# Optimization experiments

Measured on AMD Instinct MI355X. Metric: run time of the kernel, lower is better.

The kernel has to match this reference:

```python
import jax, jax.numpy as jnp
import numpy as np

EPS = 1e-5
B, N, NODE_DIM, D, H, DK, FF, L = 16, 512, 2, 256, 8, 32, 512, 3


def _u(key, shape):
    s = 1.0 / np.sqrt(shape[-1])
    return jax.random.uniform(key, shape, minval=-s, maxval=s, dtype=jnp.float32)


def _bn(h, g, b):
    # BatchNorm1d in training mode over flattened (B*N, D): biased variance
    m = h.mean(axis=(0, 1))
    v = h.var(axis=(0, 1))
    return (h - m) / jnp.sqrt(v + EPS) * g + b


def _edge_bias(em, eW1, eb1, eW2, eb2, eW3, eb3):
    # MLP(1, [16,16,H]) applied to each scalar edge weight -> (H, B, N, N)
    e = em[..., None]                       # (B,N,N,1)
    t = jax.nn.relu(e @ eW1 + eb1)          # (B,N,N,16)
    t = jax.nn.relu(t @ eW2 + eb2)          # (B,N,N,16)
    t = t @ eW3 + eb3                       # (B,N,N,H)
    return jnp.transpose(t, (3, 0, 1, 2))   # (H,B,N,N)


def _mha(h, Wq, Wk, Wv, Wo, bias):
    dk = Wq.shape[-1]
    Q = jnp.einsum('bnd,hdk->hbnk', h, Wq)
    K = jnp.einsum('bnd,hdk->hbnk', h, Wk)
    V = jnp.einsum('bnd,hdk->hbnk', h, Wv)
    scores = jnp.einsum('hbqk,hbnk->hbqn', Q, K) * (1.0 / jnp.sqrt(jnp.asarray(dk, h.dtype)))
    if bias is not None:
        scores = scores + bias
    attn = jax.nn.softmax(scores, axis=-1)
    heads = jnp.einsum('hbqn,hbnk->hbqk', attn, V)
    return jnp.einsum('hbqk,hke->bqe', heads, Wo)


def setup_inputs() -> dict:
    key = jax.random.key(0)
    ks = jax.random.split(key, 24)
    inp = {
        'x': jax.random.normal(ks[0], (B, N, NODE_DIM), dtype=jnp.float32),
        'edge_matrix': jax.random.uniform(ks[1], (B, N, N), dtype=jnp.float32),
        'init_W': _u(ks[2], (NODE_DIM, D)),
        'init_b': _u(ks[3], (D,)),
        'Wq': _u(ks[4], (L, H, D, DK)),
        'Wk': _u(ks[5], (L, H, D, DK)),
        'Wv': _u(ks[6], (L, H, D, DK)),
        'Wo': _u(ks[7], (L, H, DK, D)),
        'eW1': _u(ks[8], (1, 16)),
        'eb1': _u(ks[9], (16,)),
        'eW2': _u(ks[10], (16, 16)),
        'eb2': _u(ks[11], (16,)),
        'eW3': _u(ks[12], (16, H)),
        'eb3': _u(ks[13], (H,)),
        'bn1_g': jnp.ones((L, D), jnp.float32),
        'bn1_b': jnp.zeros((L, D), jnp.float32),
        'ffW1': _u(ks[14], (L, D, FF)),
        'ffb1': _u(ks[15], (L, FF)),
        'ffW2': _u(ks[16], (L, FF, D)),
        'ffb2': _u(ks[17], (L, D)),
        'bn2_g': jnp.ones((L, D), jnp.float32),
        'bn2_b': jnp.zeros((L, D), jnp.float32),
    }
    return inp


def reference(x, edge_matrix, init_W, init_b, Wq, Wk, Wv, Wo,
              eW1, eb1, eW2, eb2, eW3, eb3,
              bn1_g, bn1_b, ffW1, ffb1, ffW2, ffb2, bn2_g, bn2_b):
    h = x @ init_W + init_b                          # init_embed: (B,N,D)
    bias0 = _edge_bias(edge_matrix, eW1, eb1, eW2, eb2, eW3, eb3)
    for l in range(L):
        b_l = bias0 if l < 1 else None               # n_edge_encode_layers = 1
        h = h + _mha(h, Wq[l], Wk[l], Wv[l], Wo[l], b_l)
        h = _bn(h, bn1_g[l], bn1_b[l])
        h = h + (jax.nn.relu(h @ ffW1[l] + ffb1[l]) @ ffW2[l] + ffb2[l])
        h = _bn(h, bn2_g[l], bn2_b[l])
    graph_embed = h.mean(axis=1)                     # add_graph_dim == 0
    return (h, graph_embed)
```

## Files before the change

### kernel.cpp

```cpp
#include <hip/hip_runtime.h>

#define BB    16
#define NNN   512
#define DDIM  256
#define HH    8
#define DKK   32
#define FFF   512
#define MROWS 8192
#define LUTN  4096

using u16    = unsigned short;
using bf16x8 = __attribute__((ext_vector_type(8))) short;
using f32x4  = __attribute__((ext_vector_type(4))) float;

__device__ __forceinline__ float bf2f(u16 u) { return __uint_as_float(((unsigned)u) << 16); }
__device__ __forceinline__ u16 f2bf(float f) {
    unsigned u = __float_as_uint(f);
    return (u16)((u + 0x7fffu + ((u >> 16) & 1u)) >> 16);
}

__global__ __launch_bounds__(256) void init_embed_kernel(
    const float* __restrict__ x, const float* __restrict__ W,
    const float* __restrict__ b, float* __restrict__ h)
{
    size_t row = blockIdx.x;
    int c = threadIdx.x;
    float x0 = x[row * 2 + 0], x1 = x[row * 2 + 1];
    h[row * DDIM + c] = x0 * W[c] + x1 * W[DDIM + c] + b[c];
}

__global__ __launch_bounds__(256) void build_lut_kernel(
    const float* __restrict__ eW1, const float* __restrict__ eb1,
    const float* __restrict__ eW2, const float* __restrict__ eb2,
    const float* __restrict__ eW3, const float* __restrict__ eb3,
    float* __restrict__ lut)
{
    int i = blockIdx.x * 256 + threadIdx.x;
    if (i > LUTN) return;
    float e = (float)i * (1.0f / LUTN);
    float t1[16], t2[16];
    #pragma unroll
    for (int a = 0; a < 16; ++a) t1[a] = fmaxf(e * eW1[a] + eb1[a], 0.0f);
    #pragma unroll
    for (int j = 0; j < 16; ++j) {
        float s = eb2[j];
        #pragma unroll
        for (int a = 0; a < 16; ++a) s += t1[a] * eW2[a * 16 + j];
        t2[j] = fmaxf(s, 0.0f);
    }
    #pragma unroll
    for (int hd = 0; hd < 8; ++hd) {
        float s = eb3[hd];
        #pragma unroll
        for (int j = 0; j < 16; ++j) s += t2[j] * eW3[j * 8 + hd];
        lut[(size_t)i * 8 + hd] = s;
    }
}

__global__ __launch_bounds__(256) void edge_bias_kernel(
    const float* __restrict__ edge, const float* __restrict__ lut,
    u16* __restrict__ bout)
{
    size_t idx = (size_t)blockIdx.x * 256 + threadIdx.x;
    float e = edge[idx];
    float f = e * (float)LUTN;
    f = fminf(fmaxf(f, 0.0f), (float)LUTN - 0.0001f);
    int i0 = (int)f;
    float fr = f - (float)i0;
    const float4* r = (const float4*)(lut + (size_t)i0 * 8);
    float4 a0 = r[0], a1 = r[1], b0 = r[2], b1 = r[3];
    float o[8];
    o[0] = a0.x + fr * (b0.x - a0.x);
    o[1] = a0.y + fr * (b0.y - a0.y);
    o[2] = a0.z + fr * (b0.z - a0.z);
    o[3] = a0.w + fr * (b0.w - a0.w);
    o[4] = a1.x + fr * (b1.x - a1.x);
    o[5] = a1.y + fr * (b1.y - a1.y);
    o[6] = a1.z + fr * (b1.z - a1.z);
    o[7] = a1.w + fr * (b1.w - a1.w);
    #pragma unroll
    for (int hd = 0; hd < 8; ++hd)
        bout[(size_t)hd * (size_t)BB * NNN * NNN + idx] = f2bf(o[hd]);
}

#define GBM 128
#define GBN 64
#define GBK 32
#define LPAD 40

template <int BMODE>
__global__ __launch_bounds__(256) void gemm_kernel(
    const float* __restrict__ A, int lda,
    const float* __restrict__ Bp, int ldb,
    const float* __restrict__ Wq, const float* __restrict__ Wk,
    const float* __restrict__ Wv, int layer,
    float* __restrict__ C, int ldc,
    const float* __restrict__ bias, int relu,
    const float* __restrict__ res, int ldr,
    int K)
{
    __shared__ u16 Ash[GBM][LPAD];
    __shared__ u16 Asl[GBM][LPAD];
    __shared__ u16 Bsh[GBN][LPAD];
    __shared__ u16 Bsl[GBN][LPAD];
    int m0 = blockIdx.y * GBM;
    int n0 = blockIdx.x * GBN;
    int tid = threadIdx.x;
    int lid = tid & 63, wid = tid >> 6;
    int wm = wid >> 1, wn = wid & 1;
    int l15 = lid & 15, l4 = lid >> 4;

    f32x4 acc[4][2] = {};

    for (int k0 = 0; k0 < K; k0 += GBK) {
        #pragma unroll
        for (int j = 0; j < 4; ++j) {
            int idx = tid + 256 * j;
            int row = idx >> 3, k4 = idx & 7;
            float4 v = *(const float4*)(A + (size_t)(m0 + row) * lda + k0 + k4 * 4);
            ushort4 wh, wl;
            wh.x = f2bf(v.x); wl.x = f2bf(v.x - bf2f(wh.x));
            wh.y = f2bf(v.y); wl.y = f2bf(v.y - bf2f(wh.y));
            wh.z = f2bf(v.z); wl.z = f2bf(v.z - bf2f(wh.z));
            wh.w = f2bf(v.w); wl.w = f2bf(v.w - bf2f(wh.w));
            *(ushort4*)&Ash[row][k4 * 4] = wh;
            *(ushort4*)&Asl[row][k4 * 4] = wl;
        }
        #pragma unroll
        for (int j = 0; j < 8; ++j) {
            int idx = tid + 256 * j;
            int kk = idx >> 6, nn = idx & 63;
            int gk = k0 + kk, gn = n0 + nn;
            float v;
            if (BMODE == 0) {
                v = Bp[(size_t)gk * ldb + gn];
            } else {
                int mat = gn >> 8, c8 = gn & 255, hd = c8 >> 5, dk = c8 & 31;
                const float* Wsel = (mat == 0) ? Wq : ((mat == 1) ? Wk : Wv);
                v = Wsel[(((size_t)layer * HH + hd) * DDIM + gk) * DKK + dk];
            }
            u16 hh = f2bf(v);
            Bsh[nn][kk] = hh;
            Bsl[nn][kk] = f2bf(v - bf2f(hh));
        }
        __syncthreads();
        bf16x8 afh[4], afl[4], bfh[2], bfl[2];
        #pragma unroll
        for (int mi = 0; mi < 4; ++mi) {
            afh[mi] = *(const bf16x8*)&Ash[wm * 64 + mi * 16 + l15][l4 * 8];
            afl[mi] = *(const bf16x8*)&Asl[wm * 64 + mi * 16 + l15][l4 * 8];
        }
        #pragma unroll
        for (int ni = 0; ni < 2; ++ni) {
            bfh[ni] = *(const bf16x8*)&Bsh[wn * 32 + ni * 16 + l15][l4 * 8];
            bfl[ni] = *(const bf16x8*)&Bsl[wn * 32 + ni * 16 + l15][l4 * 8];
        }
        #pragma unroll
        for (int mi = 0; mi < 4; ++mi)
            #pragma unroll
            for (int ni = 0; ni < 2; ++ni) {
                acc[mi][ni] = __builtin_amdgcn_mfma_f32_16x16x32_bf16(
                    afh[mi], bfh[ni], acc[mi][ni], 0, 0, 0);
                acc[mi][ni] = __builtin_amdgcn_mfma_f32_16x16x32_bf16(
                    afh[mi], bfl[ni], acc[mi][ni], 0, 0, 0);
                acc[mi][ni] = __builtin_amdgcn_mfma_f32_16x16x32_bf16(
                    afl[mi], bfh[ni], acc[mi][ni], 0, 0, 0);
            }
        __syncthreads();
    }
    #pragma unroll
    for (int mi = 0; mi < 4; ++mi) {
        #pragma unroll
        for (int ni = 0; ni < 2; ++ni) {
            #pragma unroll
            for (int r = 0; r < 4; ++r) {
                int row = m0 + wm * 64 + mi * 16 + l4 * 4 + r;
                int col = n0 + wn * 32 + ni * 16 + l15;
                float v = acc[mi][ni][r];
                if (bias) v += bias[col];
                if (relu) v = fmaxf(v, 0.0f);
                if (res)  v += res[(size_t)row * ldr + col];
                C[(size_t)row * ldc + col] = v;
            }
        }
    }
}

__global__ __launch_bounds__(512, 2) void attn_mfma_kernel(
    const float* __restrict__ qkv, const u16* __restrict__ bias,
    float* __restrict__ att)
{
    __shared__ u16 Ksh[512][32];
    __shared__ u16 Ksl[512][32];
    __shared__ u16 Vt[32][520];
    __shared__ u16 Pw[8][16][136];
    int wg = blockIdx.x;
    int logical = (wg & 7) * 64 + (wg >> 3);
    int qt = logical & 3, hd = (logical >> 2) & 7, b = logical >> 5;
    int tid = threadIdx.x, lid = tid & 63, w = tid >> 6;
    int l15 = lid & 15, l4 = lid >> 4;

    const float* base = qkv + (size_t)b * 512 * 768;
    for (int idx = tid; idx < 512 * 32; idx += 512) {
        int n = idx >> 5, k = idx & 31;
        float kv = base[(size_t)n * 768 + 256 + hd * 32 + k];
        u16 kh = f2bf(kv);
        Ksh[n][k] = kh;
        Ksl[n][k] = f2bf(kv - bf2f(kh));
        Vt[k][n] = f2bf(base[(size_t)n * 768 + 512 + hd * 32 + k]);
    }
    __syncthreads();

    int qw0 = qt * 128 + w * 16;
    bf16x8 afh, afl;
    {
        const float* qrow = base + (size_t)(qw0 + l15) * 768 + hd * 32 + l4 * 8;
        u16 th[8], tl[8];
        #pragma unroll
        for (int j = 0; j < 8; ++j) {
            float v = qrow[j];
            th[j] = f2bf(v);
            tl[j] = f2bf(v - bf2f(th[j]));
        }
        afh = *(bf16x8*)th;
        afl = *(bf16x8*)tl;
    }

    f32x4 acc[32];
    #pragma unroll
    for (int ct = 0; ct < 32; ++ct) {
        bf16x8 bh = *(const bf16x8*)&Ksh[ct * 16 + l15][l4 * 8];
        bf16x8 bl = *(const bf16x8*)&Ksl[ct * 16 + l15][l4 * 8];
        f32x4 z = {0.0f, 0.0f, 0.0f, 0.0f};
        z = __builtin_amdgcn_mfma_f32_16x16x32_bf16(afh, bh, z, 0, 0, 0);
        z = __builtin_amdgcn_mfma_f32_16x16x32_bf16(afl, bh, z, 0, 0, 0);
        acc[ct] = __builtin_amdgcn_mfma_f32_16x16x32_bf16(afh, bl, z, 0, 0, 0);
    }

    const float scale = 0.17677669529663687f;
    if (bias) {
        size_t brow = (((size_t)hd * BB + b) * NNN + qw0 + l4 * 4) * NNN + l15;
        #pragma unroll
        for (int ct = 0; ct < 32; ++ct)
            #pragma unroll
            for (int r = 0; r < 4; ++r)
                acc[ct][r] = acc[ct][r] * scale +
                             bf2f(bias[brow + (size_t)r * NNN + ct * 16]);
    } else {
        #pragma unroll
        for (int ct = 0; ct < 32; ++ct)
            #pragma unroll
            for (int r = 0; r < 4; ++r)
                acc[ct][r] *= scale;
    }

    float linv[4];
    #pragma unroll
    for (int r = 0; r < 4; ++r) {
        float m = acc[0][r];
        #pragma unroll
        for (int ct = 1; ct < 32; ++ct) m = fmaxf(m, acc[ct][r]);
        #pragma unroll
        for (int msk = 1; msk < 16; msk <<= 1) m = fmaxf(m, __shfl_xor(m, msk));
        float lsum = 0.0f;
        #pragma unroll
        for (int ct = 0; ct < 32; ++ct) {
            float p = __expf(acc[ct][r] - m);
            acc[ct][r] = p;
            lsum += p;
        }
        #pragma unroll
        for (int msk = 1; msk < 16; msk <<= 1) lsum += __shfl_xor(lsum, msk);
        linv[r] = 1.0f / lsum;
    }

    f32x4 oacc[2] = {};
    for (int cc = 0; cc < 4; ++cc) {
        #pragma unroll
        for (int ct8 = 0; ct8 < 8; ++ct8) {
            int ct = cc * 8 + ct8;
            #pragma unroll
            for (int r = 0; r < 4; ++r)
                Pw[w][l4 * 4 + r][ct8 * 16 + l15] = f2bf(acc[ct][r]);
        }
        #pragma unroll
        for (int ks = 0; ks < 4; ++ks) {
            bf16x8 pa = *(const bf16x8*)&Pw[w][l15][ks * 32 + l4 * 8];
            #pragma unroll
            for (int ct2 = 0; ct2 < 2; ++ct2) {
                bf16x8 vb = *(const bf16x8*)&Vt[ct2 * 16 + l15][cc * 128 + ks * 32 + l4 * 8];
                oacc[ct2] = __builtin_amdgcn_mfma_f32_16x16x32_bf16(pa, vb, oacc[ct2], 0, 0, 0);
            }
        }
    }
    #pragma unroll
    for (int ct2 = 0; ct2 < 2; ++ct2)
        #pragma unroll
        for (int r = 0; r < 4; ++r)
            att[((size_t)b * NNN + qw0 + l4 * 4 + r) * DDIM + hd * 32 + ct2 * 16 + l15] =
                oacc[ct2][r] * linv[r];
}

__global__ void zero_stats_kernel(float* stats)
{
    stats[threadIdx.x] = 0.0f;
    stats[256 + threadIdx.x] = 0.0f;
}

__global__ __launch_bounds__(256) void bn_stats_kernel(
    const float* __restrict__ X, float* __restrict__ stats)
{
    int c = threadIdx.x;
    size_t r0 = (size_t)blockIdx.x * 32;
    float s = 0.0f, ss = 0.0f;
    for (int r = 0; r < 32; ++r) {
        float v = X[(r0 + r) * DDIM + c];
        s += v; ss += v * v;
    }
    atomicAdd(&stats[c], s);
    atomicAdd(&stats[256 + c], ss);
}

__global__ __launch_bounds__(256) void bn_apply_kernel(
    const float* __restrict__ X, float* __restrict__ Y,
    const float* __restrict__ stats,
    const float* __restrict__ g, const float* __restrict__ bb)
{
    int c = threadIdx.x;
    float mean = stats[c] * (1.0f / MROWS);
    float var  = stats[256 + c] * (1.0f / MROWS) - mean * mean;
    float inv  = rsqrtf(var + 1e-5f);
    float gg = g[c] * inv;
    float off = bb[c] - mean * gg;
    size_t r0 = (size_t)blockIdx.x * 8;
    #pragma unroll
    for (int r = 0; r < 8; ++r) {
        size_t o = (r0 + r) * DDIM + c;
        Y[o] = X[o] * gg + off;
    }
}

__global__ __launch_bounds__(256) void graph_embed_kernel(
    const float* __restrict__ outh, float* __restrict__ outg)
{
    int c = threadIdx.x, b = blockIdx.x;
    float s = 0.0f;
    for (int n = 0; n < NNN; ++n)
        s += outh[((size_t)b * NNN + n) * DDIM + c];
    outg[b * DDIM + c] = s * (1.0f / NNN);
}

extern "C" void kernel_launch(void* const* d_in, const int* in_sizes, int n_in,
                              void* d_out, int out_size, void* d_ws, size_t ws_size,
                              hipStream_t stream)
{
    const float* x     = (const float*)d_in[0];
    const float* edge  = (const float*)d_in[1];
    const float* initW = (const float*)d_in[2];
    const float* initb = (const float*)d_in[3];
    const float* Wq    = (const float*)d_in[4];
    const float* Wk    = (const float*)d_in[5];
    const float* Wv    = (const float*)d_in[6];
    const float* Wo    = (const float*)d_in[7];
    const float* eW1   = (const float*)d_in[8];
    const float* eb1   = (const float*)d_in[9];
    const float* eW2   = (const float*)d_in[10];
    const float* eb2   = (const float*)d_in[11];
    const float* eW3   = (const float*)d_in[12];
    const float* eb3   = (const float*)d_in[13];
    const float* bn1g  = (const float*)d_in[14];
    const float* bn1b  = (const float*)d_in[15];
    const float* ffW1  = (const float*)d_in[16];
    const float* ffb1  = (const float*)d_in[17];
    const float* ffW2  = (const float*)d_in[18];
    const float* ffb2  = (const float*)d_in[19];
    const float* bn2g  = (const float*)d_in[20];
    const float* bn2b  = (const float*)d_in[21];

    char* ws = (char*)d_ws;
    float* h     = (float*)(ws);
    float* h2    = (float*)(ws + ((size_t)8 << 20));
    float* qkv   = (float*)(ws + ((size_t)16 << 20));
    float* attb  = (float*)(ws + ((size_t)40 << 20));
    float* ff    = (float*)(ws + ((size_t)48 << 20));
    float* stats = (float*)(ws + ((size_t)64 << 20));
    float* lut   = (float*)(ws + ((size_t)64 << 20) + 4096);
    u16*   bias  = (u16*)  (ws + ((size_t)65 << 20));
    float* outh  = (float*)d_out;
    float* outg  = outh + (size_t)MROWS * DDIM;

    init_embed_kernel<<<MROWS, 256, 0, stream>>>(x, initW, initb, h);
    build_lut_kernel<<<17, 256, 0, stream>>>(eW1, eb1, eW2, eb2, eW3, eb3, lut);
    edge_bias_kernel<<<(BB * NNN * NNN) / 256, 256, 0, stream>>>(edge, lut, bias);

    for (int l = 0; l < 3; ++l) {
        gemm_kernel<1><<<dim3(768 / GBN, MROWS / GBM), 256, 0, stream>>>(
            h, 256, nullptr, 0, Wq, Wk, Wv, l, qkv, 768,
            nullptr, 0, nullptr, 0, 256);
        attn_mfma_kernel<<<512, 512, 0, stream>>>(
            qkv, (l == 0) ? bias : (const u16*)nullptr, attb);
        gemm_kernel<0><<<dim3(256 / GBN, MROWS / GBM), 256, 0, stream>>>(
            attb, 256, Wo + (size_t)l * 256 * 256, 256,
            nullptr, nullptr, nullptr, 0, h2, 256,
            nullptr, 0, h, 256, 256);
        zero_stats_kernel<<<1, 256, 0, stream>>>(stats);
        bn_stats_kernel<<<256, 256, 0, stream>>>(h2, stats);
        bn_apply_kernel<<<1024, 256, 0, stream>>>(h2, h, stats, bn1g + l * 256, bn1b + l * 256);
        gemm_kernel<0><<<dim3(512 / GBN, MROWS / GBM), 256, 0, stream>>>(
            h, 256, ffW1 + (size_t)l * 256 * 512, 512,
            nullptr, nullptr, nullptr, 0, ff, 512,
            ffb1 + l * 512, 1, nullptr, 0, 256);
        gemm_kernel<0><<<dim3(256 / GBN, MROWS / GBM), 256, 0, stream>>>(
            ff, 512, ffW2 + (size_t)l * 512 * 256, 256,
            nullptr, nullptr, nullptr, 0, h2, 256,
            ffb2 + l * 256, 0, h, 256, 512);
        zero_stats_kernel<<<1, 256, 0, stream>>>(stats);
        bn_stats_kernel<<<256, 256, 0, stream>>>(h2, stats);
        bn_apply_kernel<<<1024, 256, 0, stream>>>(
            h2, (l == 2) ? outh : h, stats, bn2g + l * 256, bn2b + l * 256);
    }
    graph_embed_kernel<<<BB, 256, 0, stream>>>(outh, outg);
}
```

Before: 779.7 us.

## Pre-split activations and weights into bf16 hi/lo planes produced by upstream kernels

Producers (init embed, GEMM epilogues, attention output, BN apply) now write activations as separate bf16 hi/lo planes, and a one-time kernel pre-splits and transposes all weights into a K-contiguous bf16 layout. The new GEMM loads A as bf16 vectors into shared memory with a K tile of 64 and reads B fragments straight from global memory, so the repeated fp32-to-split conversion and the scalar B loads in every GEMM tile disappear. Attention reads the pre-split Q/K/V and reuses one shared buffer for Ksl and the P tiles, cutting LDS use. The cost is extra global writes of hi/lo planes and B reads from global/L2 in the GEMM without shared-memory staging.

```diff
diff --git a/kernel.cpp b/kernel.cpp
--- a/kernel.cpp
+++ b/kernel.cpp
@@ -21,12 +21,57 @@
 
 __global__ __launch_bounds__(256) void init_embed_kernel(
     const float* __restrict__ x, const float* __restrict__ W,
-    const float* __restrict__ b, float* __restrict__ h)
+    const float* __restrict__ b, float* __restrict__ h,
+    u16* __restrict__ hhi, u16* __restrict__ hlo)
 {
     size_t row = blockIdx.x;
     int c = threadIdx.x;
     float x0 = x[row * 2 + 0], x1 = x[row * 2 + 1];
-    h[row * DDIM + c] = x0 * W[c] + x1 * W[DDIM + c] + b[c];
+    float v = x0 * W[c] + x1 * W[DDIM + c] + b[c];
+    size_t o = row * DDIM + c;
+    h[o] = v;
+    u16 hv = f2bf(v);
+    hhi[o] = hv;
+    hlo[o] = f2bf(v - bf2f(hv));
+}
+
+#define WT_LSTR 1048576
+__global__ __launch_bounds__(256) void wsplit_kernel(
+    const float* __restrict__ Wq, const float* __restrict__ Wk,
+    const float* __restrict__ Wv, const float* __restrict__ Wo,
+    const float* __restrict__ ffW1, const float* __restrict__ ffW2,
+    u16* __restrict__ Wt)
+{
+    int fid = blockIdx.x * 256 + threadIdx.x;
+    int l = fid >> 19, r = fid & 524287;
+    u16* base = Wt + (size_t)l * WT_LSTR;
+    float v; int off_hi, off_lo;
+    if (r < 196608) {
+        int n = r >> 8, k = r & 255;
+        int mat = n >> 8, hd = (n & 255) >> 5, dk = n & 31;
+        const float* Wsel = (mat == 0) ? Wq : ((mat == 1) ? Wk : Wv);
+        v = Wsel[(((size_t)l * HH + hd) * DDIM + k) * DKK + dk];
+        off_hi = r; off_lo = r + 196608;
+    } else if (r < 262144) {
+        int r2 = r - 196608;
+        int n = r2 >> 8, k = r2 & 255;
+        int hd = k >> 5, dk = k & 31;
+        v = Wo[(((size_t)l * HH + hd) * DKK + dk) * DDIM + n];
+        off_hi = 393216 + r2; off_lo = 458752 + r2;
+    } else if (r < 393216) {
+        int r3 = r - 262144;
+        int n = r3 >> 8, k = r3 & 255;
+        v = ffW1[((size_t)l * DDIM + k) * FFF + n];
+        off_hi = 524288 + r3; off_lo = 655360 + r3;
+    } else {
+        int r4 = r - 393216;
+        int n = r4 >> 9, k = r4 & 511;
+        v = ffW2[((size_t)l * FFF + k) * DDIM + n];
+        off_hi = 786432 + r4; off_lo = 917504 + r4;
+    }
+    u16 hv = f2bf(v);
+    base[off_hi] = hv;
+    base[off_lo] = f2bf(v - bf2f(hv));
 }
 
 __global__ __launch_bounds__(256) void build_lut_kernel(
@@ -83,89 +128,61 @@
         bout[(size_t)hd * (size_t)BB * NNN * NNN + idx] = f2bf(o[hd]);
 }
 
-#define GBM 128
-#define GBN 64
-#define GBK 32
-#define LPAD 40
-
-template <int BMODE>
-__global__ __launch_bounds__(256) void gemm_kernel(
-    const float* __restrict__ A, int lda,
-    const float* __restrict__ Bp, int ldb,
-    const float* __restrict__ Wq, const float* __restrict__ Wk,
-    const float* __restrict__ Wv, int layer,
-    float* __restrict__ C, int ldc,
+__global__ __launch_bounds__(256, 4) void gemm2_kernel(
+    const u16* __restrict__ Ah_g, const u16* __restrict__ Al_g, int K,
+    const u16* __restrict__ Bth, const u16* __restrict__ Btl, int N,
+    float* __restrict__ Cf,
+    u16* __restrict__ Chi, u16* __restrict__ Clo,
     const float* __restrict__ bias, int relu,
-    const float* __restrict__ res, int ldr,
-    int K)
-{
-    __shared__ u16 Ash[GBM][LPAD];
-    __shared__ u16 Asl[GBM][LPAD];
-    __shared__ u16 Bsh[GBN][LPAD];
-    __shared__ u16 Bsl[GBN][LPAD];
-    int m0 = blockIdx.y * GBM;
-    int n0 = blockIdx.x * GBN;
-    int tid = threadIdx.x;
-    int lid = tid & 63, wid = tid >> 6;
+    const float* __restrict__ res)
+{
+    __shared__ __align__(16) u16 Ah[128][72];
+    __shared__ __align__(16) u16 Al[128][72];
+    int m0 = blockIdx.y * 128, n0 = blockIdx.x * 64;
+    int tid = threadIdx.x, lid = tid & 63, wid = tid >> 6;
     int wm = wid >> 1, wn = wid & 1;
     int l15 = lid & 15, l4 = lid >> 4;
 
     f32x4 acc[4][2] = {};
 
-    for (int k0 = 0; k0 < K; k0 += GBK) {
+    for (int k0 = 0; k0 < K; k0 += 64) {
         #pragma unroll
         for (int j = 0; j < 4; ++j) {
-            int idx = tid + 256 * j;
-            int row = idx >> 3, k4 = idx & 7;
-            float4 v = *(const float4*)(A + (size_t)(m0 + row) * lda + k0 + k4 * 4);
-            ushort4 wh, wl;
-            wh.x = f2bf(v.x); wl.x = f2bf(v.x - bf2f(wh.x));
-            wh.y = f2bf(v.y); wl.y = f2bf(v.y - bf2f(wh.y));
-            wh.z = f2bf(v.z); wl.z = f2bf(v.z - bf2f(wh.z));
-            wh.w = f2bf(v.w); wl.w = f2bf(v.w - bf2f(wh.w));
-            *(ushort4*)&Ash[row][k4 * 4] = wh;
-            *(ushort4*)&Asl[row][k4 * 4] = wl;
-        }
-        #pragma unroll
-        for (int j = 0; j < 8; ++j) {
-            int idx = tid + 256 * j;
-            int kk = idx >> 6, nn = idx & 63;
-            int gk = k0 + kk, gn = n0 + nn;
-            float v;
-            if (BMODE == 0) {
-                v = Bp[(size_t)gk * ldb + gn];
-            } else {
-                int mat = gn >> 8, c8 = gn & 255, hd = c8 >> 5, dk = c8 & 31;
-                const float* Wsel = (mat == 0) ? Wq : ((mat == 1) ? Wk : Wv);
-                v = Wsel[(((size_t)layer * HH + hd) * DDIM + gk) * DKK + dk];
+            int c = tid + 256 * j;
+            int row = c >> 3, col8 = c & 7;
+            bf16x8 vh = *(const bf16x8*)&Ah_g[(size_t)(m0 + row) * K + k0 + col8 * 8];
+            bf16x8 vl = *(const bf16x8*)&Al_g[(size_t)(m0 + row) * K + k0 + col8 * 8];
+            *(bf16x8*)&Ah[row][col8 * 8] = vh;
+            *(bf16x8*)&Al[row][col8 * 8] = vl;
+        }
+        __syncthreads();
+        #pragma unroll
+        for (int ks = 0; ks < 2; ++ks) {
+            int ko = ks * 32;
+            bf16x8 afh[4], afl[4], bfh[2], bfl[2];
+            #pragma unroll
+            for (int mi = 0; mi < 4; ++mi) {
+                afh[mi] = *(const bf16x8*)&Ah[wm * 64 + mi * 16 + l15][ko + l4 * 8];
+                afl[mi] = *(const bf16x8*)&Al[wm * 64 + mi * 16 + l15][ko + l4 * 8];
             }
-            u16 hh = f2bf(v);
-            Bsh[nn][kk] = hh;
-            Bsl[nn][kk] = f2bf(v - bf2f(hh));
-        }
-        __syncthreads();
-        bf16x8 afh[4], afl[4], bfh[2], bfl[2];
-        #pragma unroll
-        for (int mi = 0; mi < 4; ++mi) {
-            afh[mi] = *(const bf16x8*)&Ash[wm * 64 + mi * 16 + l15][l4 * 8];
-            afl[mi] = *(const bf16x8*)&Asl[wm * 64 + mi * 16 + l15][l4 * 8];
-        }
-        #pragma unroll
-        for (int ni = 0; ni < 2; ++ni) {
-            bfh[ni] = *(const bf16x8*)&Bsh[wn * 32 + ni * 16 + l15][l4 * 8];
-            bfl[ni] = *(const bf16x8*)&Bsl[wn * 32 + ni * 16 + l15][l4 * 8];
-        }
-        #pragma unroll
-        for (int mi = 0; mi < 4; ++mi)
             #pragma unroll
             for (int ni = 0; ni < 2; ++ni) {
-                acc[mi][ni] = __builtin_amdgcn_mfma_f32_16x16x32_bf16(
-                    afh[mi], bfh[ni], acc[mi][ni], 0, 0, 0);
-                acc[mi][ni] = __builtin_amdgcn_mfma_f32_16x16x32_bf16(
-                    afh[mi], bfl[ni], acc[mi][ni], 0, 0, 0);
-                acc[mi][ni] = __builtin_amdgcn_mfma_f32_16x16x32_bf16(
-                    afl[mi], bfh[ni], acc[mi][ni], 0, 0, 0);
+                size_t brow = (size_t)(n0 + wn * 32 + ni * 16 + l15) * K + k0 + ko + l4 * 8;
+                bfh[ni] = *(const bf16x8*)&Bth[brow];
+                bfl[ni] = *(const bf16x8*)&Btl[brow];
             }
+            #pragma unroll
+            for (int mi = 0; mi < 4; ++mi)
+                #pragma unroll
+                for (int ni = 0; ni < 2; ++ni) {
+                    acc[mi][ni] = __builtin_amdgcn_mfma_f32_16x16x32_bf16(
+                        afh[mi], bfh[ni], acc[mi][ni], 0, 0, 0);
+                    acc[mi][ni] = __builtin_amdgcn_mfma_f32_16x16x32_bf16(
+                        afh[mi], bfl[ni], acc[mi][ni], 0, 0, 0);
+                    acc[mi][ni] = __builtin_amdgcn_mfma_f32_16x16x32_bf16(
+                        afl[mi], bfh[ni], acc[mi][ni], 0, 0, 0);
+                }
+        }
         __syncthreads();
     }
     #pragma unroll
@@ -179,52 +196,54 @@
                 float v = acc[mi][ni][r];
                 if (bias) v += bias[col];
                 if (relu) v = fmaxf(v, 0.0f);
-                if (res)  v += res[(size_t)row * ldr + col];
-                C[(size_t)row * ldc + col] = v;
+                if (res)  v += res[(size_t)row * N + col];
+                size_t o = (size_t)row * N + col;
+                if (Cf) Cf[o] = v;
+                if (Chi) {
+                    u16 hv = f2bf(v);
+                    Chi[o] = hv;
+                    Clo[o] = f2bf(v - bf2f(hv));
+                }
             }
         }
     }
 }
 
 __global__ __launch_bounds__(512, 2) void attn_mfma_kernel(
-    const float* __restrict__ qkv, const u16* __restrict__ bias,
-    float* __restrict__ att)
-{
-    __shared__ u16 Ksh[512][32];
-    __shared__ u16 Ksl[512][32];
-    __shared__ u16 Vt[32][520];
-    __shared__ u16 Pw[8][16][136];
+    const u16* __restrict__ qkv_hi, const u16* __restrict__ qkv_lo,
+    const u16* __restrict__ bias,
+    u16* __restrict__ attb_hi, u16* __restrict__ attb_lo)
+{
+    __shared__ __align__(16) u16 Ksh[512][40];
+    __shared__ __align__(16) u16 UB[512 * 40];
+    __shared__ __align__(16) u16 Vt[32][520];
     int wg = blockIdx.x;
     int logical = (wg & 7) * 64 + (wg >> 3);
     int qt = logical & 3, hd = (logical >> 2) & 7, b = logical >> 5;
     int tid = threadIdx.x, lid = tid & 63, w = tid >> 6;
     int l15 = lid & 15, l4 = lid >> 4;
 
-    const float* base = qkv + (size_t)b * 512 * 768;
-    for (int idx = tid; idx < 512 * 32; idx += 512) {
-        int n = idx >> 5, k = idx & 31;
-        float kv = base[(size_t)n * 768 + 256 + hd * 32 + k];
-        u16 kh = f2bf(kv);
-        Ksh[n][k] = kh;
-        Ksl[n][k] = f2bf(kv - bf2f(kh));
-        Vt[k][n] = f2bf(base[(size_t)n * 768 + 512 + hd * 32 + k]);
+    const u16* baseh = qkv_hi + (size_t)b * 512 * 768;
+    const u16* basel = qkv_lo + (size_t)b * 512 * 768;
+    u16 (*Ksl)[40] = (u16(*)[40])UB;
+
+    for (int q4 = tid; q4 < 512 * 8; q4 += 512) {
+        int n = q4 >> 3, c4 = q4 & 7;
+        ushort4 kh = *(const ushort4*)&baseh[(size_t)n * 768 + 256 + hd * 32 + c4 * 4];
+        ushort4 kl = *(const ushort4*)&basel[(size_t)n * 768 + 256 + hd * 32 + c4 * 4];
+        ushort4 vh = *(const ushort4*)&baseh[(size_t)n * 768 + 512 + hd * 32 + c4 * 4];
+        *(ushort4*)&Ksh[n][c4 * 4] = kh;
+        *(ushort4*)&Ksl[n][c4 * 4] = kl;
+        Vt[c4 * 4 + 0][n] = vh.x;
+        Vt[c4 * 4 + 1][n] = vh.y;
+        Vt[c4 * 4 + 2][n] = vh.z;
+        Vt[c4 * 4 + 3][n] = vh.w;
     }
     __syncthreads();
 
     int qw0 = qt * 128 + w * 16;
-    bf16x8 afh, afl;
-    {
-        const float* qrow = base + (size_t)(qw0 + l15) * 768 + hd * 32 + l4 * 8;
-        u16 th[8], tl[8];
-        #pragma unroll
-        for (int j = 0; j < 8; ++j) {
-            float v = qrow[j];
-            th[j] = f2bf(v);
-            tl[j] = f2bf(v - bf2f(th[j]));
-        }
-        afh = *(bf16x8*)th;
-        afl = *(bf16x8*)tl;
-    }
+    bf16x8 afh = *(const bf16x8*)&baseh[(size_t)(qw0 + l15) * 768 + hd * 32 + l4 * 8];
+    bf16x8 afl = *(const bf16x8*)&basel[(size_t)(qw0 + l15) * 768 + hd * 32 + l4 * 8];
 
     f32x4 acc[32];
     #pragma unroll
@@ -236,6 +255,7 @@
         z = __builtin_amdgcn_mfma_f32_16x16x32_bf16(afl, bh, z, 0, 0, 0);
         acc[ct] = __builtin_amdgcn_mfma_f32_16x16x32_bf16(afh, bl, z, 0, 0, 0);
     }
+    __syncthreads();
 
     const float scale = 0.17677669529663687f;
     if (bias) {
@@ -274,21 +294,22 @@
         linv[r] = 1.0f / lsum;
     }
 
+    u16 (*Pw)[72] = (u16(*)[72])(UB + w * 16 * 72);
     f32x4 oacc[2] = {};
-    for (int cc = 0; cc < 4; ++cc) {
-        #pragma unroll
-        for (int ct8 = 0; ct8 < 8; ++ct8) {
-            int ct = cc * 8 + ct8;
+    for (int cc = 0; cc < 8; ++cc) {
+        #pragma unroll
+        for (int ct4 = 0; ct4 < 4; ++ct4) {
+            int ct = cc * 4 + ct4;
             #pragma unroll
             for (int r = 0; r < 4; ++r)
-                Pw[w][l4 * 4 + r][ct8 * 16 + l15] = f2bf(acc[ct][r]);
-        }
-        #pragma unroll
-        for (int ks = 0; ks < 4; ++ks) {
-            bf16x8 pa = *(const bf16x8*)&Pw[w][l15][ks * 32 + l4 * 8];
+                Pw[l4 * 4 + r][ct4 * 16 + l15] = f2bf(acc[ct][r]);
+        }
+        #pragma unroll
+        for (int ks = 0; ks < 2; ++ks) {
+            bf16x8 pa = *(const bf16x8*)&Pw[l15][ks * 32 + l4 * 8];
             #pragma unroll
             for (int ct2 = 0; ct2 < 2; ++ct2) {
-                bf16x8 vb = *(const bf16x8*)&Vt[ct2 * 16 + l15][cc * 128 + ks * 32 + l4 * 8];
+                bf16x8 vb = *(const bf16x8*)&Vt[ct2 * 16 + l15][cc * 64 + ks * 32 + l4 * 8];
                 oacc[ct2] = __builtin_amdgcn_mfma_f32_16x16x32_bf16(pa, vb, oacc[ct2], 0, 0, 0);
             }
         }
@@ -296,9 +317,13 @@
     #pragma unroll
     for (int ct2 = 0; ct2 < 2; ++ct2)
         #pragma unroll
-        for (int r = 0; r < 4; ++r)
-            att[((size_t)b * NNN + qw0 + l4 * 4 + r) * DDIM + hd * 32 + ct2 * 16 + l15] =
-                oacc[ct2][r] * linv[r];
+        for (int r = 0; r < 4; ++r) {
+            float o = oacc[ct2][r] * linv[r];
+            size_t oi = ((size_t)b * NNN + qw0 + l4 * 4 + r) * DDIM + hd * 32 + ct2 * 16 + l15;
+            u16 hv = f2bf(o);
+            attb_hi[oi] = hv;
+            attb_lo[oi] = f2bf(o - bf2f(hv));
+        }
 }
 
 __global__ void zero_stats_kernel(float* stats)
@@ -323,6 +348,7 @@
 
 __global__ __launch_bounds__(256) void bn_apply_kernel(
     const float* __restrict__ X, float* __restrict__ Y,
+    u16* __restrict__ Yhi, u16* __restrict__ Ylo,
     const float* __restrict__ stats,
     const float* __restrict__ g, const float* __restrict__ bb)
 {
@@ -336,7 +362,13 @@
     #pragma unroll
     for (int r = 0; r < 8; ++r) {
         size_t o = (r0 + r) * DDIM + c;
-        Y[o] = X[o] * gg + off;
+        float y = X[o] * gg + off;
+        Y[o] = y;
+        if (Yhi) {
+            u16 hv = f2bf(y);
+            Yhi[o] = hv;
+            Ylo[o] = f2bf(y - bf2f(hv));
+        }
     }
 }
 
@@ -378,46 +410,56 @@
     const float* bn2b  = (const float*)d_in[21];
 
     char* ws = (char*)d_ws;
-    float* h     = (float*)(ws);
-    float* h2    = (float*)(ws + ((size_t)8 << 20));
-    float* qkv   = (float*)(ws + ((size_t)16 << 20));
-    float* attb  = (float*)(ws + ((size_t)40 << 20));
-    float* ff    = (float*)(ws + ((size_t)48 << 20));
-    float* stats = (float*)(ws + ((size_t)64 << 20));
-    float* lut   = (float*)(ws + ((size_t)64 << 20) + 4096);
-    u16*   bias  = (u16*)  (ws + ((size_t)65 << 20));
+    float* h      = (float*)(ws);
+    float* h2     = (float*)(ws + ((size_t)8  << 20));
+    u16*   h_hi   = (u16*)  (ws + ((size_t)16 << 20));
+    u16*   h_lo   = (u16*)  (ws + ((size_t)20 << 20));
+    u16*   qkv_hi = (u16*)  (ws + ((size_t)24 << 20));
+    u16*   qkv_lo = (u16*)  (ws + ((size_t)36 << 20));
+    float* stats  = (float*)(ws + ((size_t)48 << 20));
+    float* lut    = (float*)(ws + ((size_t)48 << 20) + 4096);
+    u16*   Wt     = (u16*)  (ws + ((size_t)49 << 20));
+    u16*   bias   = (u16*)  (ws + ((size_t)56 << 20));
+    u16*   attb_hi = h_hi;
+    u16*   attb_lo = h_lo;
+    u16*   ff_hi   = qkv_hi;
+    u16*   ff_lo   = qkv_lo;
     float* outh  = (float*)d_out;
     float* outg  = outh + (size_t)MROWS * DDIM;
 
-    init_embed_kernel<<<MROWS, 256, 0, stream>>>(x, initW, initb, h);
+    wsplit_kernel<<<6144, 256, 0, stream>>>(Wq, Wk, Wv, Wo, ffW1, ffW2, Wt);
+    init_embed_kernel<<<MROWS, 256, 0, stream>>>(x, initW, initb, h, h_hi, h_lo);
     build_lut_kernel<<<17, 256, 0, stream>>>(eW1, eb1, eW2, eb2, eW3, eb3, lut);
     edge_bias_kernel<<<(BB * NNN * NNN) / 256, 256, 0, stream>>>(edge, lut, bias);
 
     for (int l = 0; l < 3; ++l) {
-        gemm_kernel<1><<<dim3(768 / GBN, MROWS / GBM), 256, 0, stream>>>(
-            h, 256, nullptr, 0, Wq, Wk, Wv, l, qkv, 768,
-            nullptr, 0, nullptr, 0, 256);
+        u16* WL = Wt + (size_t)l * WT_LSTR;
+        gemm2_kernel<<<dim3(12, 64), 256, 0, stream>>>(
+            h_hi, h_lo, 256, WL, WL + 196608, 768,
+            nullptr, qkv_hi, qkv_lo, nullptr, 0, nullptr);
         attn_mfma_kernel<<<512, 512, 0, stream>>>(
-            qkv, (l == 0) ? bias : (const u16*)nullptr, attb);
-        gemm_kernel<0><<<dim3(256 / GBN, MROWS / GBM), 256, 0, stream>>>(
-            attb, 256, Wo + (size_t)l * 256 * 256, 256,
-            nullptr, nullptr, nullptr, 0, h2, 256,
-            nullptr, 0, h, 256, 256);
-        zero_stats_kernel<<<1, 256, 0, stream>>>(stats);
-        bn_stats_kernel<<<256, 256, 0, stream>>>(h2, stats);
-        bn_apply_kernel<<<1024, 256, 0, stream>>>(h2, h, stats, bn1g + l * 256, bn1b + l * 256);
-        gemm_kernel<0><<<dim3(512 / GBN, MROWS / GBM), 256, 0, stream>>>(
-            h, 256, ffW1 + (size_t)l * 256 * 512, 512,
-            nullptr, nullptr, nullptr, 0, ff, 512,
-            ffb1 + l * 512, 1, nullptr, 0, 256);
-        gemm_kernel<0><<<dim3(256 / GBN, MROWS / GBM), 256, 0, stream>>>(
-            ff, 512, ffW2 + (size_t)l * 512 * 256, 256,
-            nullptr, nullptr, nullptr, 0, h2, 256,
-            ffb2 + l * 256, 0, h, 256, 512);
+            qkv_hi, qkv_lo, (l == 0) ? bias : (const u16*)nullptr, attb_hi, attb_lo);
+        gemm2_kernel<<<dim3(4, 64), 256, 0, stream>>>(
+            attb_hi, attb_lo, 256, WL + 393216, WL + 458752, 256,
+            h2, nullptr, nullptr, nullptr, 0, h);
         zero_stats_kernel<<<1, 256, 0, stream>>>(stats);
         bn_stats_kernel<<<256, 256, 0, stream>>>(h2, stats);
         bn_apply_kernel<<<1024, 256, 0, stream>>>(
-            h2, (l == 2) ? outh : h, stats, bn2g + l * 256, bn2b + l * 256);
+            h2, h, h_hi, h_lo, stats, bn1g + l * 256, bn1b + l * 256);
+        gemm2_kernel<<<dim3(8, 64), 256, 0, stream>>>(
+            h_hi, h_lo, 256, WL + 524288, WL + 655360, 512,
+            nullptr, ff_hi, ff_lo, ffb1 + l * 512, 1, nullptr);
+        gemm2_kernel<<<dim3(4, 64), 256, 0, stream>>>(
+            ff_hi, ff_lo, 512, WL + 786432, WL + 917504, 256,
+            h2, nullptr, nullptr, ffb2 + l * 256, 0, h);
+        zero_stats_kernel<<<1, 256, 0, stream>>>(stats);
+        bn_stats_kernel<<<256, 256, 0, stream>>>(h2, stats);
+        if (l == 2)
+            bn_apply_kernel<<<1024, 256, 0, stream>>>(
+                h2, outh, nullptr, nullptr, stats, bn2g + l * 256, bn2b + l * 256);
+        else
+            bn_apply_kernel<<<1024, 256, 0, stream>>>(
+                h2, h, h_hi, h_lo, stats, bn2g + l * 256, bn2b + l * 256);
     }
     graph_embed_kernel<<<BB, 256, 0, stream>>>(outh, outg);
 }
```

Measured after the change: 759.0 us. 2.6% less time.
